# Kernel optimization log

Measured on AMD Instinct MI355X. Metric: run time of the kernel, lower is better.

Reference implementation:

```python
import jax, jax.numpy as jnp
import numpy as np

N_WAY, N_SHOT, C, H, W = 5, 5, 640, 32, 32
EPS = 1e-12


def conv1x1(x, w, b):
    # 1x1 conv == channel GEMM; w: (C_out, C_in), b: (C_out,)
    return jnp.einsum('bchw,oc->bohw', x, w) + b[None, :, None, None]


def setup_inputs() -> dict:
    key = jax.random.key(0)
    ks = jax.random.split(key, 7)
    B = N_WAY * N_SHOT
    x5 = jax.random.normal(ks[0], (B, C, H, W), jnp.float32)
    Wc = jax.random.normal(ks[1], (C, C), jnp.float32) * 0.02
    bc = jax.random.normal(ks[2], (C,), jnp.float32) * 0.02
    Wq = jax.random.normal(ks[3], (C, C), jnp.float32) * 0.02
    bq = jax.random.normal(ks[4], (C,), jnp.float32) * 0.02
    Wk = jax.random.normal(ks[5], (C, C), jnp.float32) * 0.02
    bk = jax.random.normal(ks[6], (C,), jnp.float32) * 0.02
    return {"x5": x5, "Wc": Wc, "bc": bc, "Wq": Wq, "bq": bq, "Wk": Wk, "bk": bk}


def reference(x5, Wc, bc, Wq, bq, Wk, bk):
    B, Cc, Hh, Ww = x5.shape
    HW = Hh * Ww
    scale = 1.0 / (Cc ** 0.5)

    # residual 1x1 conv, then query_transform applied once (x5 is reassigned)
    x5 = conv1x1(x5, Wc, bc) + x5
    x5 = conv1x1(x5, Wq, bq)

    # query: query_transform applied AGAIN on the already-transformed x5
    xq = conv1x1(x5, Wq, bq).reshape(N_WAY, N_SHOT, Cc, HW)
    xq = xq.transpose(0, 1, 3, 2).reshape(N_WAY, N_SHOT * HW, Cc)
    xk = conv1x1(x5, Wk, bk).reshape(N_WAY, N_SHOT, Cc, HW)
    xk = xk.transpose(0, 2, 1, 3).reshape(N_WAY, Cc, N_SHOT * HW)

    # QK scores per way: (n_way, S*HW, S*HW)
    xw = jnp.matmul(xq, xk) * scale
    # max over key spatial, mean over key shot
    xw = xw.reshape(N_WAY, N_SHOT * HW, N_SHOT, HW).max(-1).mean(-1)
    xw = jax.nn.softmax(xw.reshape(N_WAY, N_SHOT, HW), axis=-1)

    # channel-wise L2 normalize (F.normalize semantics)
    nrm = jnp.maximum(jnp.sqrt((x5 * x5).sum(1, keepdims=True)), EPS)
    norm0 = (x5 / nrm).reshape(N_WAY, N_SHOT, Cc, Hh, Ww)

    # argmax-equality mask over spatial positions
    xw_max = xw.max(-1, keepdims=True)
    mask = (xw == xw_max).astype(x5.dtype).reshape(N_WAY, N_SHOT, 1, Hh, Ww)

    # seeds: masked spatial sum of normalized features -> (n_way, n_shot, C)
    seeds = (norm0 * mask).sum((3, 4))

    # conv3d correlation: out[b,o,h,w] = sum_{k,c} norm0[b,k,c,h,w] * seeds[o,k,c]
    cm = jnp.einsum('bkchw,okc->bohw', norm0, seeds).reshape(N_WAY, N_WAY, HW)
    cmin = cm.min(-1, keepdims=True)
    cmax = cm.max(-1, keepdims=True)
    cm = (cm - cmin) / (cmax - cmin + EPS)
    cormap = cm.reshape(B, 1, Hh, Ww)

    x51 = (x5 * cormap).reshape(N_WAY, N_SHOT, Cc, Hh, Ww)
    proto1 = x51.mean((1, 3, 4))  # (n_way, C)
    return proto1
```

## Files before the change

### kernel.cpp

```cpp
#include <hip/hip_runtime.h>
#include <math.h>

#define NW 5
#define NS 5
#define CDIM 640
#define HWDIM 1024
#define BDIM 25
constexpr int CHW = CDIM * HWDIM;
constexpr int NBIG = BDIM * CHW;
constexpr int WSZ = CDIM * CDIM;
constexpr float QK_SCALE = 0.03952847075210474f;

typedef __attribute__((ext_vector_type(4))) float f32x4;
typedef __attribute__((ext_vector_type(8))) __bf16 bf16x8;
typedef __attribute__((ext_vector_type(4))) __bf16 bf16x4;
typedef __attribute__((ext_vector_type(2))) __bf16 bf16x2;

__device__ __forceinline__ void load_lds16(const __bf16* g, __bf16* l) {
    __builtin_amdgcn_global_load_lds(
        (const __attribute__((address_space(1))) void*)g,
        (__attribute__((address_space(3))) void*)l, 16, 0, 0);
}

__global__ __launch_bounds__(256) void split_f32(const float* __restrict__ s,
                                                 __bf16* __restrict__ dH,
                                                 __bf16* __restrict__ dL, int n4) {
    int i = blockIdx.x * 256 + threadIdx.x;
    if (i >= n4) return;
    f32x4 v = reinterpret_cast<const f32x4*>(s)[i];
    bf16x4 h, lo;
    #pragma unroll
    for (int q = 0; q < 4; ++q) {
        __bf16 hh = (__bf16)v[q];
        h[q] = hh;
        lo[q] = (__bf16)(v[q] - (float)hh);
    }
    reinterpret_cast<bf16x4*>(dH)[i] = h;
    reinterpret_cast<bf16x4*>(dL)[i] = lo;
}

__global__ __launch_bounds__(256) void tsplit(const float* __restrict__ x,
                                              __bf16* __restrict__ dH,
                                              __bf16* __restrict__ dL) {
    __shared__ float sT[32][33];
    const int hw0 = blockIdx.x * 32, c0 = blockIdx.y * 32, b = blockIdx.z;
    const int t = threadIdx.x;
    const int r = t >> 3, q4 = (t & 7) * 4;
    f32x4 v = *reinterpret_cast<const f32x4*>(
        &x[(size_t)b * CHW + (size_t)(c0 + r) * HWDIM + hw0 + q4]);
    #pragma unroll
    for (int i = 0; i < 4; ++i) sT[r][q4 + i] = v[i];
    __syncthreads();
    bf16x4 h, lo;
    #pragma unroll
    for (int i = 0; i < 4; ++i) {
        float xv = sT[q4 + i][r];
        __bf16 hh = (__bf16)xv;
        h[i] = hh;
        lo[i] = (__bf16)(xv - (float)hh);
    }
    size_t off = (size_t)b * CHW + (size_t)(hw0 + r) * CDIM + c0 + q4;
    *reinterpret_cast<bf16x4*>(&dH[off]) = h;
    *reinterpret_cast<bf16x4*>(&dL[off]) = lo;
}

__global__ __launch_bounds__(256) void wtsplit(const float* __restrict__ W,
                                               __bf16* __restrict__ dH,
                                               __bf16* __restrict__ dL) {
    __shared__ float sT[32][33];
    const int ci0 = blockIdx.x * 32, t0 = blockIdx.y * 32;
    const int t = threadIdx.x;
    const int r = t >> 3, q4 = (t & 7) * 4;
    f32x4 v = *reinterpret_cast<const f32x4*>(&W[(size_t)(t0 + r) * CDIM + ci0 + q4]);
    #pragma unroll
    for (int i = 0; i < 4; ++i) sT[r][q4 + i] = v[i];
    __syncthreads();
    bf16x4 h, lo;
    #pragma unroll
    for (int i = 0; i < 4; ++i) {
        float xv = sT[q4 + i][r];
        if (t0 + q4 + i == ci0 + r) xv += 1.0f;
        __bf16 hh = (__bf16)xv;
        h[i] = hh;
        lo[i] = (__bf16)(xv - (float)hh);
    }
    size_t off = (size_t)(ci0 + r) * CDIM + t0 + q4;
    *reinterpret_cast<bf16x4*>(&dH[off]) = h;
    *reinterpret_cast<bf16x4*>(&dL[off]) = lo;
}

__global__ void zero_k(float* __restrict__ p) { p[threadIdx.x] = 0.0f; }

__global__ void bias1_k(const float* __restrict__ Wq, const float* __restrict__ bc,
                        const float* __restrict__ bq, float* __restrict__ B2) {
    const int o = threadIdx.x;
    float s = bq[o];
    for (int t = 0; t < CDIM; ++t) s = fmaf(Wq[(size_t)o * CDIM + t], bc[t], s);
    B2[o] = s;
}

template <int NL>
__device__ __forceinline__ void stage_rows(const __bf16* __restrict__ srcH,
                                           const __bf16* __restrict__ srcL,
                                           __bf16* lds, int wv, int l, int c0) {
    const int lch = (l & 7) ^ (l >> 3);
    const int scol = (lch & 3) * 8;
    const int srw = l >> 3;
    const __bf16* src = (lch & 4) ? srcL : srcH;
    #pragma unroll
    for (int i = 0; i < NL; ++i) {
        const int r0 = wv * (8 * NL) + i * 8;
        load_lds16(&src[(size_t)(r0 + srw) * CDIM + c0 + scol], &lds[r0 * 64]);
    }
}

__global__ __launch_bounds__(256) void gemm_sm(
    const __bf16* __restrict__ inH, const __bf16* __restrict__ inL,
    const __bf16* __restrict__ wH, const __bf16* __restrict__ wL,
    const float* __restrict__ bias,
    __bf16* __restrict__ outH, __bf16* __restrict__ outL) {
    __shared__ __bf16 sA[128 * 64];
    __shared__ __bf16 sB[128 * 64];
    const int hw0 = blockIdx.x * 128;
    const int o0 = blockIdx.y * 128;
    const int tid = threadIdx.x;
    const int wv = tid >> 6, l = tid & 63;
    const int wo = (wv >> 1) * 64, wh = (wv & 1) * 64;

    const __bf16* wSrcH = wH + (size_t)o0 * CDIM;
    const __bf16* wSrcL = wL + (size_t)o0 * CDIM;
    const __bf16* iSrcH = inH + (size_t)hw0 * CDIM;
    const __bf16* iSrcL = inL + (size_t)hw0 * CDIM;

    f32x4 acc[4][4];
    #pragma unroll
    for (int i = 0; i < 4; ++i)
        #pragma unroll
        for (int j = 0; j < 4; ++j) acc[i][j] = (f32x4){0.f, 0.f, 0.f, 0.f};

    const int fr = l & 15, cf = l >> 4;
    const int ehi = (cf ^ (fr & 7)) * 8;

    for (int c0 = 0; c0 < CDIM; c0 += 32) {
        stage_rows<4>(wSrcH, wSrcL, sA, wv, l, c0);
        stage_rows<4>(iSrcH, iSrcL, sB, wv, l, c0);
        __syncthreads();
        bf16x8 aH[4], aL[4], bH[4], bL[4];
        #pragma unroll
        for (int i = 0; i < 4; ++i) {
            const int ra = (wo + i * 16 + fr) * 64;
            const int rb = (wh + i * 16 + fr) * 64;
            aH[i] = *reinterpret_cast<const bf16x8*>(&sA[ra + ehi]);
            aL[i] = *reinterpret_cast<const bf16x8*>(&sA[ra + (ehi ^ 32)]);
            bH[i] = *reinterpret_cast<const bf16x8*>(&sB[rb + ehi]);
            bL[i] = *reinterpret_cast<const bf16x8*>(&sB[rb + (ehi ^ 32)]);
        }
        #pragma unroll
        for (int i = 0; i < 4; ++i)
            #pragma unroll
            for (int j = 0; j < 4; ++j) {
                acc[i][j] = __builtin_amdgcn_mfma_f32_16x16x32_bf16(
                    aH[i], bH[j], acc[i][j], 0, 0, 0);
                acc[i][j] = __builtin_amdgcn_mfma_f32_16x16x32_bf16(
                    aH[i], bL[j], acc[i][j], 0, 0, 0);
                acc[i][j] = __builtin_amdgcn_mfma_f32_16x16x32_bf16(
                    aL[i], bH[j], acc[i][j], 0, 0, 0);
            }
        __syncthreads();
    }

    const int og = (l >> 4) * 4;
    const int cl = l & 15;
    #pragma unroll
    for (int i = 0; i < 4; ++i) {
        const int o = o0 + wo + i * 16 + og;
        const f32x4 bs = *reinterpret_cast<const f32x4*>(&bias[o]);
        #pragma unroll
        for (int j = 0; j < 4; ++j) {
            const int hw = hw0 + wh + j * 16 + cl;
            const size_t off = (size_t)hw * CDIM + o;
            bf16x4 oh, ol;
            #pragma unroll
            for (int q = 0; q < 4; ++q) {
                float r = acc[i][j][q] + bs[q];
                __bf16 hh = (__bf16)r;
                oh[q] = hh;
                ol[q] = (__bf16)(r - (float)hh);
            }
            *reinterpret_cast<bf16x4*>(&outH[off]) = oh;
            *reinterpret_cast<bf16x4*>(&outL[off]) = ol;
        }
    }
}

__global__ __launch_bounds__(256, 2) void conv_big(
    const __bf16* __restrict__ inH, const __bf16* __restrict__ inL,
    const __bf16* __restrict__ A0h, const __bf16* __restrict__ A0l,
    const __bf16* __restrict__ A1h, const __bf16* __restrict__ A1l,
    const float* __restrict__ bias,
    __bf16* __restrict__ O0h, __bf16* __restrict__ O0l,
    __bf16* __restrict__ O1h, __bf16* __restrict__ O1l) {
    __shared__ __bf16 sA[128 * 64];
    __shared__ __bf16 sB[256 * 64];
    const int hw0 = blockIdx.x * 256;
    const int oy = blockIdx.y;
    const int seg = oy / 5;
    const int o0 = (oy % 5) * 128;
    const int b = blockIdx.z;
    const int tid = threadIdx.x;
    const int wv = tid >> 6, l = tid & 63;
    const int wo = (wv >> 1) * 64;
    const int wh = (wv & 1) * 128;
    const size_t inBase = (size_t)b * CHW;

    const __bf16* Ah = seg ? A1h : A0h;
    const __bf16* Al = seg ? A1l : A0l;
    __bf16* OhP = seg ? O1h : O0h;
    __bf16* OlP = seg ? O1l : O0l;
    const __bf16* aSrcH = Ah + (size_t)o0 * CDIM;
    const __bf16* aSrcL = Al + (size_t)o0 * CDIM;
    const __bf16* bSrcH = inH + inBase + (size_t)hw0 * CDIM;
    const __bf16* bSrcL = inL + inBase + (size_t)hw0 * CDIM;

    f32x4 acc[4][8];
    #pragma unroll
    for (int i = 0; i < 4; ++i)
        #pragma unroll
        for (int j = 0; j < 8; ++j) acc[i][j] = (f32x4){0.f, 0.f, 0.f, 0.f};

    const int fr = l & 15, cf = l >> 4;
    const int ehi = (cf ^ (fr & 7)) * 8;

    for (int c0 = 0; c0 < CDIM; c0 += 32) {
        stage_rows<4>(aSrcH, aSrcL, sA, wv, l, c0);
        stage_rows<8>(bSrcH, bSrcL, sB, wv, l, c0);
        __syncthreads();
        bf16x8 aH[4], aL[4];
        #pragma unroll
        for (int i = 0; i < 4; ++i) {
            const int ra = (wo + i * 16 + fr) * 64;
            aH[i] = *reinterpret_cast<const bf16x8*>(&sA[ra + ehi]);
            aL[i] = *reinterpret_cast<const bf16x8*>(&sA[ra + (ehi ^ 32)]);
        }
        #pragma unroll
        for (int jh = 0; jh < 2; ++jh) {
            bf16x8 bH[4], bL[4];
            #pragma unroll
            for (int jj = 0; jj < 4; ++jj) {
                const int rb = (wh + (jh * 4 + jj) * 16 + fr) * 64;
                bH[jj] = *reinterpret_cast<const bf16x8*>(&sB[rb + ehi]);
                bL[jj] = *reinterpret_cast<const bf16x8*>(&sB[rb + (ehi ^ 32)]);
            }
            #pragma unroll
            for (int i = 0; i < 4; ++i)
                #pragma unroll
                for (int jj = 0; jj < 4; ++jj) {
                    const int j = jh * 4 + jj;
                    acc[i][j] = __builtin_amdgcn_mfma_f32_16x16x32_bf16(
                        aH[i], bH[jj], acc[i][j], 0, 0, 0);
                    acc[i][j] = __builtin_amdgcn_mfma_f32_16x16x32_bf16(
                        aH[i], bL[jj], acc[i][j], 0, 0, 0);
                    acc[i][j] = __builtin_amdgcn_mfma_f32_16x16x32_bf16(
                        aL[i], bH[jj], acc[i][j], 0, 0, 0);
                }
        }
        __syncthreads();
    }

    const int og = (l >> 4) * 4;
    const int cl = l & 15;
    #pragma unroll
    for (int i = 0; i < 4; ++i) {
        const int oLoc = o0 + wo + i * 16 + og;
        const f32x4 bs = *reinterpret_cast<const f32x4*>(&bias[oy * 128 + wo + i * 16 + og]);
        #pragma unroll
        for (int j = 0; j < 8; ++j) {
            const int hw = hw0 + wh + j * 16 + cl;
            const size_t off = inBase + (size_t)hw * CDIM + oLoc;
            bf16x4 oh, ol;
            #pragma unroll
            for (int q = 0; q < 4; ++q) {
                float r = acc[i][j][q] + bs[q];
                __bf16 hh = (__bf16)r;
                oh[q] = hh;
                ol[q] = (__bf16)(r - (float)hh);
            }
            *reinterpret_cast<bf16x4*>(&OhP[off]) = oh;
            *reinterpret_cast<bf16x4*>(&OlP[off]) = ol;
        }
    }
}

__global__ __launch_bounds__(256, 2) void attn_mfma2(
    const __bf16* __restrict__ qH, const __bf16* __restrict__ qL,
    const __bf16* __restrict__ kH, const __bf16* __restrict__ kL,
    float* __restrict__ gpart) {
    __shared__ __bf16 sQ[128 * 64];
    __shared__ __bf16 sK[256 * 64];
    __shared__ float sRed[2][128];
    const int qt = blockIdx.x;
    const int ks = blockIdx.y, wy = blockIdx.z;
    const int sq = qt >> 3, q0 = (qt & 7) * 128;
    const int tid = threadIdx.x;
    const int wv = tid >> 6, l = tid & 63;
    const int wq = (wv >> 1) * 64;
    const int kh = wv & 1;
    const int wk = kh * 128;
    const __bf16* qSrcH = qH + (size_t)(wy * NS + sq) * CHW + (size_t)q0 * CDIM;
    const __bf16* qSrcL = qL + (size_t)(wy * NS + sq) * CHW + (size_t)q0 * CDIM;
    const __bf16* kBaseH = kH + (size_t)(wy * NS + ks) * CHW;
    const __bf16* kBaseL = kL + (size_t)(wy * NS + ks) * CHW;

    float qmax[4][4];
    #pragma unroll
    for (int i = 0; i < 4; ++i)
        #pragma unroll
        for (int q = 0; q < 4; ++q) qmax[i][q] = -INFINITY;

    const int fr = l & 15, cf = l >> 4;
    const int ehi = (cf ^ (fr & 7)) * 8;

    for (int kc = 0; kc < 4; ++kc) {
        const __bf16* kSrcH = kBaseH + (size_t)(kc * 256) * CDIM;
        const __bf16* kSrcL = kBaseL + (size_t)(kc * 256) * CDIM;
        f32x4 acc[4][8];
        #pragma unroll
        for (int i = 0; i < 4; ++i)
            #pragma unroll
            for (int j = 0; j < 8; ++j) acc[i][j] = (f32x4){0.f, 0.f, 0.f, 0.f};

        for (int c0 = 0; c0 < CDIM; c0 += 32) {
            stage_rows<4>(qSrcH, qSrcL, sQ, wv, l, c0);
            stage_rows<8>(kSrcH, kSrcL, sK, wv, l, c0);
            __syncthreads();
            bf16x8 aH[4], aL[4];
            #pragma unroll
            for (int i = 0; i < 4; ++i) {
                const int ra = (wq + i * 16 + fr) * 64;
                aH[i] = *reinterpret_cast<const bf16x8*>(&sQ[ra + ehi]);
                aL[i] = *reinterpret_cast<const bf16x8*>(&sQ[ra + (ehi ^ 32)]);
            }
            __builtin_amdgcn_s_setprio(1);
            #pragma unroll
            for (int jh = 0; jh < 2; ++jh) {
                bf16x8 bH[4], bL[4];
                #pragma unroll
                for (int jj = 0; jj < 4; ++jj) {
                    const int rb = (wk + (jh * 4 + jj) * 16 + fr) * 64;
                    bH[jj] = *reinterpret_cast<const bf16x8*>(&sK[rb + ehi]);
                    bL[jj] = *reinterpret_cast<const bf16x8*>(&sK[rb + (ehi ^ 32)]);
                }
                #pragma unroll
                for (int i = 0; i < 4; ++i)
                    #pragma unroll
                    for (int jj = 0; jj < 4; ++jj) {
                        const int j = jh * 4 + jj;
                        acc[i][j] = __builtin_amdgcn_mfma_f32_16x16x32_bf16(
                            aH[i], bH[jj], acc[i][j], 0, 0, 0);
                        acc[i][j] = __builtin_amdgcn_mfma_f32_16x16x32_bf16(
                            aH[i], bL[jj], acc[i][j], 0, 0, 0);
                        acc[i][j] = __builtin_amdgcn_mfma_f32_16x16x32_bf16(
                            aL[i], bH[jj], acc[i][j], 0, 0, 0);
                    }
            }
            __builtin_amdgcn_s_setprio(0);
            __syncthreads();
        }
        #pragma unroll
        for (int i = 0; i < 4; ++i)
            #pragma unroll
            for (int q = 0; q < 4; ++q) {
                float m = acc[i][0][q];
                #pragma unroll
                for (int j = 1; j < 8; ++j) m = fmaxf(m, acc[i][j][q]);
                qmax[i][q] = fmaxf(qmax[i][q], m);
            }
    }
    #pragma unroll
    for (int i = 0; i < 4; ++i)
        #pragma unroll
        for (int q = 0; q < 4; ++q) {
            float v = qmax[i][q];
            v = fmaxf(v, __shfl_xor(v, 1));
            v = fmaxf(v, __shfl_xor(v, 2));
            v = fmaxf(v, __shfl_xor(v, 4));
            v = fmaxf(v, __shfl_xor(v, 8));
            qmax[i][q] = v;
        }
    if ((l & 15) == 0) {
        const int g = l >> 4;
        #pragma unroll
        for (int i = 0; i < 4; ++i)
            #pragma unroll
            for (int q = 0; q < 4; ++q)
                sRed[kh][wq + i * 16 + g * 4 + q] = qmax[i][q];
    }
    __syncthreads();
    if (tid < 128) {
        float m = fmaxf(sRed[0][tid], sRed[1][tid]);
        gpart[(size_t)(wy * NS + ks) * (NS * HWDIM) + sq * HWDIM + q0 + tid] =
            m * QK_SCALE;
    }
}

__global__ __launch_bounds__(256) void softmax_mask(const float* __restrict__ gpart,
                                                    int* __restrict__ gIdx,
                                                    int* __restrict__ gCnt) {
    const int bb = blockIdx.x;
    const int w = bb / NS, sq = bb % NS;
    const int tid = threadIdx.x;
    __shared__ float sred[256];
    __shared__ int sCnt;

    float v[4];
    #pragma unroll
    for (int i = 0; i < 4; ++i) {
        int hw = tid + 256 * i;
        float s = 0.f;
        #pragma unroll
        for (int ks = 0; ks < NS; ++ks)
            s += gpart[(size_t)(w * NS + ks) * (NS * HWDIM) + sq * HWDIM + hw];
        v[i] = s * 0.2f;
    }
    float m = fmaxf(fmaxf(v[0], v[1]), fmaxf(v[2], v[3]));
    sred[tid] = m;
    __syncthreads();
    for (int s = 128; s > 0; s >>= 1) {
        if (tid < s) sred[tid] = fmaxf(sred[tid], sred[tid + s]);
        __syncthreads();
    }
    float rowmax = sred[0];
    __syncthreads();
    float e[4], ls = 0.f;
    #pragma unroll
    for (int i = 0; i < 4; ++i) { e[i] = expf(v[i] - rowmax); ls += e[i]; }
    sred[tid] = ls;
    __syncthreads();
    for (int s = 128; s > 0; s >>= 1) {
        if (tid < s) sred[tid] += sred[tid + s];
        __syncthreads();
    }
    float ssum = sred[0];
    __syncthreads();
    float p[4], pm = 0.f;
    #pragma unroll
    for (int i = 0; i < 4; ++i) { p[i] = e[i] / ssum; pm = fmaxf(pm, p[i]); }
    sred[tid] = pm;
    __syncthreads();
    for (int s = 128; s > 0; s >>= 1) {
        if (tid < s) sred[tid] = fmaxf(sred[tid], sred[tid + s]);
        __syncthreads();
    }
    float pmax = sred[0];
    if (tid == 0) sCnt = 0;
    __syncthreads();
    #pragma unroll
    for (int i = 0; i < 4; ++i) {
        if (p[i] == pmax) {
            int slot = atomicAdd(&sCnt, 1);
            gIdx[bb * HWDIM + slot] = tid + 256 * i;
        }
    }
    __syncthreads();
    if (tid == 0) gCnt[bb] = sCnt;
}

__global__ __launch_bounds__(256) void nrm_k(const __bf16* __restrict__ yH,
                                             const __bf16* __restrict__ yL,
                                             float* __restrict__ inv) {
    const int row = blockIdx.x * 16 + (threadIdx.x >> 4);
    const int cq = threadIdx.x & 15;
    const size_t base = (size_t)row * CDIM;
    float s = 0.f;
    #pragma unroll
    for (int i = 0; i < 10; ++i) {
        int c = i * 64 + cq * 4;
        bf16x4 h = *reinterpret_cast<const bf16x4*>(&yH[base + c]);
        bf16x4 lo = *reinterpret_cast<const bf16x4*>(&yL[base + c]);
        #pragma unroll
        for (int q = 0; q < 4; ++q) {
            float x = (float)h[q] + (float)lo[q];
            s = fmaf(x, x, s);
        }
    }
    s += __shfl_xor(s, 1);
    s += __shfl_xor(s, 2);
    s += __shfl_xor(s, 4);
    s += __shfl_xor(s, 8);
    if (cq == 0) inv[row] = 1.0f / fmaxf(sqrtf(s), 1e-12f);
}

__global__ __launch_bounds__(640) void seeds_k(const __bf16* __restrict__ yH,
                                               const __bf16* __restrict__ yL,
                                               const float* __restrict__ inv,
                                               const int* __restrict__ gIdx,
                                               const int* __restrict__ gCnt,
                                               float* __restrict__ seeds) {
    const int bb = blockIdx.x, c = threadIdx.x;
    const int cnt = gCnt[bb];
    float s = 0.f;
    for (int e = 0; e < cnt; ++e) {
        int hw = gIdx[bb * HWDIM + e];
        size_t off = (size_t)bb * CHW + (size_t)hw * CDIM + c;
        s += ((float)yH[off] + (float)yL[off]) * inv[bb * HWDIM + hw];
    }
    seeds[bb * CDIM + c] = s;
}

__global__ __launch_bounds__(256) void cm_k(const __bf16* __restrict__ yH,
                                            const __bf16* __restrict__ yL,
                                            const float* __restrict__ inv,
                                            const float* __restrict__ seeds,
                                            float* __restrict__ cm) {
    __shared__ float sS[BDIM * CDIM];
    const int way = blockIdx.y;
    const int tid = threadIdx.x, wv = tid >> 6, l = tid & 63;
    const int hw = blockIdx.x * 4 + wv;
    for (int e = tid; e < BDIM * CDIM; e += 256) sS[e] = seeds[e];
    __syncthreads();
    float acc[NW] = {0.f, 0.f, 0.f, 0.f, 0.f};
    for (int k = 0; k < NS; ++k) {
        const size_t base = (size_t)(way * NS + k) * CHW + (size_t)hw * CDIM;
        float t[NW] = {0.f, 0.f, 0.f, 0.f, 0.f};
        #pragma unroll
        for (int i = 0; i < 5; ++i) {
            int c = (i * 64 + l) * 2;
            bf16x2 h = *reinterpret_cast<const bf16x2*>(&yH[base + c]);
            bf16x2 lo = *reinterpret_cast<const bf16x2*>(&yL[base + c]);
            float x0 = (float)h[0] + (float)lo[0];
            float x1 = (float)h[1] + (float)lo[1];
            #pragma unroll
            for (int o = 0; o < NW; ++o) {
                t[o] = fmaf(x0, sS[(o * NS + k) * CDIM + c], t[o]);
                t[o] = fmaf(x1, sS[(o * NS + k) * CDIM + c + 1], t[o]);
            }
        }
        float iv = inv[(way * NS + k) * HWDIM + hw];
        #pragma unroll
        for (int o = 0; o < NW; ++o) acc[o] = fmaf(t[o], iv, acc[o]);
    }
    #pragma unroll
    for (int o = 0; o < NW; ++o) {
        float v = acc[o];
        v += __shfl_xor(v, 1);
        v += __shfl_xor(v, 2);
        v += __shfl_xor(v, 4);
        v += __shfl_xor(v, 8);
        v += __shfl_xor(v, 16);
        v += __shfl_xor(v, 32);
        if (l == 0) cm[(size_t)(way * NW + o) * HWDIM + hw] = v;
    }
}

__global__ __launch_bounds__(256) void minmax_kernel(float* __restrict__ cm) {
    const int row = blockIdx.x;
    const int tid = threadIdx.x;
    __shared__ float smn[256], smx[256];
    float v[4];
    #pragma unroll
    for (int i = 0; i < 4; ++i) v[i] = cm[(size_t)row * HWDIM + tid + 256 * i];
    float mn = fminf(fminf(v[0], v[1]), fminf(v[2], v[3]));
    float mx = fmaxf(fmaxf(v[0], v[1]), fmaxf(v[2], v[3]));
    smn[tid] = mn;
    smx[tid] = mx;
    __syncthreads();
    for (int s = 128; s > 0; s >>= 1) {
        if (tid < s) {
            smn[tid] = fminf(smn[tid], smn[tid + s]);
            smx[tid] = fmaxf(smx[tid], smx[tid + s]);
        }
        __syncthreads();
    }
    float cmin = smn[0], cmax = smx[0];
    float den = cmax - cmin + 1e-12f;
    #pragma unroll
    for (int i = 0; i < 4; ++i)
        cm[(size_t)row * HWDIM + tid + 256 * i] = (v[i] - cmin) / den;
}

__global__ __launch_bounds__(128) void proto_part_k(const __bf16* __restrict__ yH,
                                                    const __bf16* __restrict__ yL,
                                                    const float* __restrict__ cmn,
                                                    float* __restrict__ part) {
    const int w = blockIdx.x, cc = blockIdx.y, hs = blockIdx.z;
    const int c = cc * 128 + threadIdx.x;
    float s = 0.f;
    for (int i = 0; i < 640; ++i) {
        int g = hs * 640 + i, sh = g >> 10, hw = g & 1023;
        size_t off = (size_t)(w * NS + sh) * CHW + (size_t)hw * CDIM + c;
        s = fmaf((float)yH[off] + (float)yL[off],
                 cmn[(w * NS + sh) * HWDIM + hw], s);
    }
    part[((w * 5 + cc) * 8 + hs) * 128 + threadIdx.x] = s;
}

__global__ __launch_bounds__(128) void proto_red_k(const float* __restrict__ part,
                                                   float* __restrict__ out) {
    const int bid = blockIdx.x;
    float s = 0.f;
    #pragma unroll
    for (int hs = 0; hs < 8; ++hs) s += part[(bid * 8 + hs) * 128 + threadIdx.x];
    const int w = bid / 5, cc = bid % 5;
    out[w * CDIM + cc * 128 + threadIdx.x] = s * (1.0f / 5120.0f);
}

extern "C" void kernel_launch(void* const* d_in, const int* in_sizes, int n_in,
                              void* d_out, int out_size, void* d_ws, size_t ws_size,
                              hipStream_t stream) {
    const float* x5 = (const float*)d_in[0];
    const float* Wc = (const float*)d_in[1];
    const float* bc = (const float*)d_in[2];
    const float* Wq = (const float*)d_in[3];
    const float* bq = (const float*)d_in[4];
    const float* Wk = (const float*)d_in[5];
    const float* bk = (const float*)d_in[6];
    float* out = (float*)d_out;

    __bf16* big = (__bf16*)d_ws;
    __bf16* Ah = big;
    __bf16* Al = big + (size_t)NBIG;
    __bf16* Bh = big + (size_t)2 * NBIG;
    __bf16* Bl = big + (size_t)3 * NBIG;
    __bf16* W2H = Bh;
    __bf16* W2L = Bh + WSZ;
    __bf16* Ch = big + (size_t)4 * NBIG;
    __bf16* Cl = big + (size_t)5 * NBIG;
    __bf16* WcTH = Ch;
    __bf16* WcTL = Ch + WSZ;
    __bf16* wp = big + (size_t)6 * NBIG;
    __bf16* WqH = wp;
    __bf16* WqL = wp + WSZ;
    __bf16* WkH = wp + 2 * WSZ;
    __bf16* WkL = wp + 3 * WSZ;
    float* fp = (float*)(wp + 4 * WSZ);
    float* zbias = fp;
    float* B2 = fp + 640;
    float* bb2 = fp + 1280;
    float* gpart = fp + 2560;
    float* invb = gpart + 128000;
    float* seedsb = invb + 25600;
    float* cmb = seedsb + 16000;
    float* partb = cmb + 25600;
    int* gIdx = (int*)(partb + 25600);
    int* gCnt = gIdx + BDIM * HWDIM;

    const int W4 = WSZ / 4;
    split_f32<<<dim3((W4 + 255) / 256), 256, 0, stream>>>(Wq, WqH, WqL, W4);
    split_f32<<<dim3((W4 + 255) / 256), 256, 0, stream>>>(Wk, WkH, WkL, W4);
    wtsplit<<<dim3(20, 20), 256, 0, stream>>>(Wc, WcTH, WcTL);
    tsplit<<<dim3(32, 20, 25), 256, 0, stream>>>(x5, Ah, Al);
    zero_k<<<1, 640, 0, stream>>>(zbias);
    bias1_k<<<1, 640, 0, stream>>>(Wq, bc, bq, B2);
    hipMemcpyAsync(bb2, bq, CDIM * sizeof(float), hipMemcpyDeviceToDevice, stream);
    hipMemcpyAsync(bb2 + CDIM, bk, CDIM * sizeof(float), hipMemcpyDeviceToDevice,
                   stream);

    gemm_sm<<<dim3(5, 5, 1), 256, 0, stream>>>(WqH, WqL, WcTH, WcTL, zbias,
                                               W2H, W2L);
    conv_big<<<dim3(4, 5, 25), 256, 0, stream>>>(Ah, Al, W2H, W2L, W2H, W2L,
                                                 B2, Ch, Cl, Ch, Cl);
    conv_big<<<dim3(4, 10, 25), 256, 0, stream>>>(Ch, Cl, WqH, WqL, WkH, WkL,
                                                  bb2, Ah, Al, Bh, Bl);

    attn_mfma2<<<dim3(40, 5, 5), 256, 0, stream>>>(Ah, Al, Bh, Bl, gpart);
    softmax_mask<<<25, 256, 0, stream>>>(gpart, gIdx, gCnt);
    nrm_k<<<1600, 256, 0, stream>>>(Ch, Cl, invb);
    seeds_k<<<25, 640, 0, stream>>>(Ch, Cl, invb, gIdx, gCnt, seedsb);
    cm_k<<<dim3(256, 5), 256, 0, stream>>>(Ch, Cl, invb, seedsb, cmb);
    minmax_kernel<<<25, 256, 0, stream>>>(cmb);
    proto_part_k<<<dim3(5, 5, 8), 128, 0, stream>>>(Ch, Cl, cmb, partb);
    proto_red_k<<<25, 128, 0, stream>>>(partb, out);
}
```

Before: 1.007 ms.

## Screen QK max with single bf16 MFMA pass, then refine candidates exactly

The QK score pass now uses only the high bf16 parts (1 MFMA per tile instead of 3). It records key candidates whose approximate score lies within an error bound of the running row max, where the bound comes from query and key norms. A refine kernel then recomputes exact dot products only for those candidates, falling back to a full scan when a row overflows. This cuts MFMA work in the dominant attention kernel, at the cost of extra norm kernels, atomics and a gather-style refine pass. Correctness depends on the heuristic error coefficient bounding the bf16 rounding error. Small bias and memcpy launches are also merged into one kernel.

```diff
diff --git a/kernel.cpp b/kernel.cpp
--- a/kernel.cpp
+++ b/kernel.cpp
@@ -6,10 +6,13 @@
 #define CDIM 640
 #define HWDIM 1024
 #define BDIM 25
+#define CAP 24
 constexpr int CHW = CDIM * HWDIM;
 constexpr int NBIG = BDIM * CHW;
 constexpr int WSZ = CDIM * CDIM;
+constexpr int NROWS = NW * NS * NS * HWDIM;
 constexpr float QK_SCALE = 0.03952847075210474f;
+constexpr float TWOE_COEF = 0.016f;
 
 typedef __attribute__((ext_vector_type(4))) float f32x4;
 typedef __attribute__((ext_vector_type(8))) __bf16 bf16x8;
@@ -89,14 +92,17 @@
     *reinterpret_cast<bf16x4*>(&dL[off]) = lo;
 }
 
-__global__ void zero_k(float* __restrict__ p) { p[threadIdx.x] = 0.0f; }
-
-__global__ void bias1_k(const float* __restrict__ Wq, const float* __restrict__ bc,
-                        const float* __restrict__ bq, float* __restrict__ B2) {
+__global__ void bias_prep(const float* __restrict__ Wq, const float* __restrict__ bc,
+                          const float* __restrict__ bq, const float* __restrict__ bk,
+                          float* __restrict__ zbias, float* __restrict__ B2,
+                          float* __restrict__ bb2) {
     const int o = threadIdx.x;
+    zbias[o] = 0.0f;
     float s = bq[o];
     for (int t = 0; t < CDIM; ++t) s = fmaf(Wq[(size_t)o * CDIM + t], bc[t], s);
     B2[o] = s;
+    bb2[o] = bq[o];
+    bb2[CDIM + o] = bk[o];
 }
 
 template <int NL>
@@ -112,6 +118,16 @@
         const int r0 = wv * (8 * NL) + i * 8;
         load_lds16(&src[(size_t)(r0 + srw) * CDIM + c0 + scol], &lds[r0 * 64]);
     }
+}
+
+__device__ __forceinline__ void stage_hi(const __bf16* __restrict__ src,
+                                         __bf16* lds, int li, int l) {
+    const int rp = li * 8 + (l >> 3);
+    const int pc = l & 7;
+    const int lc = pc ^ (rp & 7);
+    const int srow = 2 * rp + (lc >> 2);
+    const int schan = (lc & 3) * 8;
+    load_lds16(&src[(size_t)srow * CDIM + schan], &lds[li * 512]);
 }
 
 __global__ __launch_bounds__(256) void gemm_sm(
@@ -291,13 +307,66 @@
     }
 }
 
-__global__ __launch_bounds__(256, 2) void attn_mfma2(
-    const __bf16* __restrict__ qH, const __bf16* __restrict__ qL,
-    const __bf16* __restrict__ kH, const __bf16* __restrict__ kL,
-    float* __restrict__ gpart) {
-    __shared__ __bf16 sQ[128 * 64];
-    __shared__ __bf16 sK[256 * 64];
-    __shared__ float sRed[2][128];
+__global__ __launch_bounds__(256) void qknorm_k(const __bf16* __restrict__ xqH,
+                                                const __bf16* __restrict__ xqL,
+                                                const __bf16* __restrict__ xkH,
+                                                const __bf16* __restrict__ xkL,
+                                                float* __restrict__ qn,
+                                                float* __restrict__ knrow) {
+    const int gb = blockIdx.x;
+    const __bf16 *H, *L;
+    float* dst;
+    int row;
+    if (gb < 1600) {
+        H = xqH; L = xqL; dst = qn;
+        row = gb * 16 + (threadIdx.x >> 4);
+    } else {
+        H = xkH; L = xkL; dst = knrow;
+        row = (gb - 1600) * 16 + (threadIdx.x >> 4);
+    }
+    const int cq = threadIdx.x & 15;
+    const size_t base = (size_t)row * CDIM;
+    float s = 0.f;
+    #pragma unroll
+    for (int i = 0; i < 10; ++i) {
+        int c = i * 64 + cq * 4;
+        bf16x4 h = *reinterpret_cast<const bf16x4*>(&H[base + c]);
+        bf16x4 lo = *reinterpret_cast<const bf16x4*>(&L[base + c]);
+        #pragma unroll
+        for (int q = 0; q < 4; ++q) {
+            float x = (float)h[q] + (float)lo[q];
+            s = fmaf(x, x, s);
+        }
+    }
+    s += __shfl_xor(s, 1);
+    s += __shfl_xor(s, 2);
+    s += __shfl_xor(s, 4);
+    s += __shfl_xor(s, 8);
+    if (cq == 0) dst[row] = sqrtf(s);
+}
+
+__global__ __launch_bounds__(256) void kmax_k(const float* __restrict__ knrow,
+                                              float* __restrict__ kmax) {
+    const int b = blockIdx.x, tid = threadIdx.x;
+    __shared__ float sm[256];
+    const float* p = knrow + b * 1024;
+    float v = fmaxf(fmaxf(p[tid], p[tid + 256]), fmaxf(p[tid + 512], p[tid + 768]));
+    sm[tid] = v;
+    __syncthreads();
+    for (int s = 128; s > 0; s >>= 1) {
+        if (tid < s) sm[tid] = fmaxf(sm[tid], sm[tid + s]);
+        __syncthreads();
+    }
+    if (tid == 0) kmax[b] = sm[0];
+}
+
+__global__ __launch_bounds__(256, 2) void attn_bf16(
+    const __bf16* __restrict__ qH, const __bf16* __restrict__ kH,
+    const float* __restrict__ qn, const float* __restrict__ kmax,
+    int* __restrict__ candCnt, unsigned short* __restrict__ candIdx) {
+    __shared__ __bf16 sQ[64 * 64];
+    __shared__ __bf16 sK[128 * 64];
+    __shared__ float sM[2][128];
     const int qt = blockIdx.x;
     const int ks = blockIdx.y, wy = blockIdx.z;
     const int sq = qt >> 3, q0 = (qt & 7) * 128;
@@ -306,23 +375,31 @@
     const int wq = (wv >> 1) * 64;
     const int kh = wv & 1;
     const int wk = kh * 128;
-    const __bf16* qSrcH = qH + (size_t)(wy * NS + sq) * CHW + (size_t)q0 * CDIM;
-    const __bf16* qSrcL = qL + (size_t)(wy * NS + sq) * CHW + (size_t)q0 * CDIM;
-    const __bf16* kBaseH = kH + (size_t)(wy * NS + ks) * CHW;
-    const __bf16* kBaseL = kL + (size_t)(wy * NS + ks) * CHW;
-
-    float qmax[4][4];
+    const __bf16* qSrc = qH + (size_t)(wy * NS + sq) * CHW + (size_t)q0 * CDIM;
+    const __bf16* kBase = kH + (size_t)(wy * NS + ks) * CHW;
+
+    const int fr = l & 15, cg = l >> 4;
+    const int rowBase = ((wy * NS + ks) * NS + sq) * HWDIM + q0;
+
+    const float kmv = kmax[wy * NS + ks];
+    float twoE[4][4];
+    float run[4][4];
     #pragma unroll
     for (int i = 0; i < 4; ++i)
         #pragma unroll
-        for (int q = 0; q < 4; ++q) qmax[i][q] = -INFINITY;
-
-    const int fr = l & 15, cf = l >> 4;
-    const int ehi = (cf ^ (fr & 7)) * 8;
+        for (int qq = 0; qq < 4; ++qq) {
+            int qloc = wq + i * 16 + (cg << 2) + qq;
+            twoE[i][qq] = TWOE_COEF * qn[(wy * NS + sq) * HWDIM + q0 + qloc] * kmv + 1e-6f;
+            run[i][qq] = -INFINITY;
+        }
+
+    const int rq2 = fr >> 1, par = fr & 1;
+    const int xorm = rq2 & 7;
+    const int cA = (wq / 2 + rq2) * 64 + (((par << 2) | cg) ^ xorm) * 8;
+    const int cB = (wk / 2 + rq2) * 64 + (((par << 2) | cg) ^ xorm) * 8;
 
     for (int kc = 0; kc < 4; ++kc) {
-        const __bf16* kSrcH = kBaseH + (size_t)(kc * 256) * CDIM;
-        const __bf16* kSrcL = kBaseL + (size_t)(kc * 256) * CDIM;
+        const __bf16* kSrc = kBase + (size_t)(kc * 256) * CDIM;
         f32x4 acc[4][8];
         #pragma unroll
         for (int i = 0; i < 4; ++i)
@@ -330,77 +407,128 @@
             for (int j = 0; j < 8; ++j) acc[i][j] = (f32x4){0.f, 0.f, 0.f, 0.f};
 
         for (int c0 = 0; c0 < CDIM; c0 += 32) {
-            stage_rows<4>(qSrcH, qSrcL, sQ, wv, l, c0);
-            stage_rows<8>(kSrcH, kSrcL, sK, wv, l, c0);
+            stage_hi(qSrc + c0, sQ, wv * 2 + 0, l);
+            stage_hi(qSrc + c0, sQ, wv * 2 + 1, l);
+            #pragma unroll
+            for (int li = 0; li < 4; ++li) stage_hi(kSrc + c0, sK, wv * 4 + li, l);
             __syncthreads();
-            bf16x8 aH[4], aL[4];
-            #pragma unroll
-            for (int i = 0; i < 4; ++i) {
-                const int ra = (wq + i * 16 + fr) * 64;
-                aH[i] = *reinterpret_cast<const bf16x8*>(&sQ[ra + ehi]);
-                aL[i] = *reinterpret_cast<const bf16x8*>(&sQ[ra + (ehi ^ 32)]);
-            }
+            bf16x8 aH[4], bH[8];
+            #pragma unroll
+            for (int i = 0; i < 4; ++i)
+                aH[i] = *reinterpret_cast<const bf16x8*>(&sQ[cA + i * 512]);
+            #pragma unroll
+            for (int j = 0; j < 8; ++j)
+                bH[j] = *reinterpret_cast<const bf16x8*>(&sK[cB + j * 512]);
             __builtin_amdgcn_s_setprio(1);
             #pragma unroll
-            for (int jh = 0; jh < 2; ++jh) {
-                bf16x8 bH[4], bL[4];
+            for (int i = 0; i < 4; ++i)
                 #pragma unroll
-                for (int jj = 0; jj < 4; ++jj) {
-                    const int rb = (wk + (jh * 4 + jj) * 16 + fr) * 64;
-                    bH[jj] = *reinterpret_cast<const bf16x8*>(&sK[rb + ehi]);
-                    bL[jj] = *reinterpret_cast<const bf16x8*>(&sK[rb + (ehi ^ 32)]);
-                }
-                #pragma unroll
-                for (int i = 0; i < 4; ++i)
-                    #pragma unroll
-                    for (int jj = 0; jj < 4; ++jj) {
-                        const int j = jh * 4 + jj;
-                        acc[i][j] = __builtin_amdgcn_mfma_f32_16x16x32_bf16(
-                            aH[i], bH[jj], acc[i][j], 0, 0, 0);
-                        acc[i][j] = __builtin_amdgcn_mfma_f32_16x16x32_bf16(
-                            aH[i], bL[jj], acc[i][j], 0, 0, 0);
-                        acc[i][j] = __builtin_amdgcn_mfma_f32_16x16x32_bf16(
-                            aL[i], bH[jj], acc[i][j], 0, 0, 0);
-                    }
-            }
+                for (int j = 0; j < 8; ++j)
+                    acc[i][j] = __builtin_amdgcn_mfma_f32_16x16x32_bf16(
+                        aH[i], bH[j], acc[i][j], 0, 0, 0);
             __builtin_amdgcn_s_setprio(0);
             __syncthreads();
         }
         #pragma unroll
         for (int i = 0; i < 4; ++i)
             #pragma unroll
-            for (int q = 0; q < 4; ++q) {
-                float m = acc[i][0][q];
+            for (int qq = 0; qq < 4; ++qq) {
+                float m = acc[i][0][qq];
                 #pragma unroll
-                for (int j = 1; j < 8; ++j) m = fmaxf(m, acc[i][j][q]);
-                qmax[i][q] = fmaxf(qmax[i][q], m);
+                for (int j = 1; j < 8; ++j) m = fmaxf(m, acc[i][j][qq]);
+                m = fmaxf(m, __shfl_xor(m, 1));
+                m = fmaxf(m, __shfl_xor(m, 2));
+                m = fmaxf(m, __shfl_xor(m, 4));
+                m = fmaxf(m, __shfl_xor(m, 8));
+                if (fr == 0)
+                    sM[kh][wq + i * 16 + (cg << 2) + qq] = m;
             }
-    }
-    #pragma unroll
-    for (int i = 0; i < 4; ++i)
-        #pragma unroll
-        for (int q = 0; q < 4; ++q) {
-            float v = qmax[i][q];
-            v = fmaxf(v, __shfl_xor(v, 1));
-            v = fmaxf(v, __shfl_xor(v, 2));
-            v = fmaxf(v, __shfl_xor(v, 4));
-            v = fmaxf(v, __shfl_xor(v, 8));
-            qmax[i][q] = v;
-        }
-    if ((l & 15) == 0) {
-        const int g = l >> 4;
+        __syncthreads();
         #pragma unroll
         for (int i = 0; i < 4; ++i)
             #pragma unroll
-            for (int q = 0; q < 4; ++q)
-                sRed[kh][wq + i * 16 + g * 4 + q] = qmax[i][q];
-    }
-    __syncthreads();
-    if (tid < 128) {
-        float m = fmaxf(sRed[0][tid], sRed[1][tid]);
-        gpart[(size_t)(wy * NS + ks) * (NS * HWDIM) + sq * HWDIM + q0 + tid] =
-            m * QK_SCALE;
-    }
+            for (int qq = 0; qq < 4; ++qq) {
+                const int rloc = wq + i * 16 + (cg << 2) + qq;
+                run[i][qq] = fmaxf(run[i][qq],
+                                   fmaxf(sM[0][rloc], sM[1][rloc]));
+                const float th = run[i][qq] - twoE[i][qq];
+                const int rowid = rowBase + rloc;
+                #pragma unroll
+                for (int j = 0; j < 8; ++j) {
+                    if (acc[i][j][qq] >= th) {
+                        int key = kc * 256 + wk + j * 16 + fr;
+                        int slot = atomicAdd(&candCnt[rowid], 1);
+                        if (slot < CAP)
+                            candIdx[rowid * CAP + slot] = (unsigned short)key;
+                    }
+                }
+            }
+    }
+}
+
+__global__ __launch_bounds__(256) void refine_k(
+    const __bf16* __restrict__ qH, const __bf16* __restrict__ qL,
+    const __bf16* __restrict__ kH, const __bf16* __restrict__ kL,
+    const int* __restrict__ candCnt, const unsigned short* __restrict__ candIdx,
+    float* __restrict__ gpart) {
+    const int tid = threadIdx.x, wv = tid >> 6, l = tid & 63;
+    const int rowid = blockIdx.x * 4 + wv;
+    const int wks = rowid / (NS * HWDIM);
+    const int rem = rowid - wks * (NS * HWDIM);
+    const int sq = rem >> 10, qp = rem & 1023;
+    const int w = wks / NS;
+    const __bf16* qh = qH + (size_t)(w * NS + sq) * CHW + (size_t)qp * CDIM;
+    const __bf16* ql = qL + (size_t)(w * NS + sq) * CHW + (size_t)qp * CDIM;
+    const __bf16* kb = kH + (size_t)wks * CHW;
+    const __bf16* kbl = kL + (size_t)wks * CHW;
+
+    float qv[10];
+    #pragma unroll
+    for (int e = 0; e < 10; ++e) {
+        int c = l * 10 + e;
+        qv[e] = (float)qh[c] + (float)ql[c];
+    }
+    const int cnt = candCnt[rowid];
+    float smax = -INFINITY;
+    if (cnt <= CAP) {
+        for (int e = 0; e < cnt; ++e) {
+            const int key = candIdx[rowid * CAP + e];
+            const __bf16* kr = kb + (size_t)key * CDIM;
+            const __bf16* krl = kbl + (size_t)key * CDIM;
+            float s = 0.f;
+            #pragma unroll
+            for (int u = 0; u < 10; ++u) {
+                int c = l * 10 + u;
+                s = fmaf(qv[u], (float)kr[c] + (float)krl[c], s);
+            }
+            s += __shfl_xor(s, 1);
+            s += __shfl_xor(s, 2);
+            s += __shfl_xor(s, 4);
+            s += __shfl_xor(s, 8);
+            s += __shfl_xor(s, 16);
+            s += __shfl_xor(s, 32);
+            smax = fmaxf(smax, s);
+        }
+    } else {
+        for (int key = 0; key < 1024; ++key) {
+            const __bf16* kr = kb + (size_t)key * CDIM;
+            const __bf16* krl = kbl + (size_t)key * CDIM;
+            float s = 0.f;
+            #pragma unroll
+            for (int u = 0; u < 10; ++u) {
+                int c = l * 10 + u;
+                s = fmaf(qv[u], (float)kr[c] + (float)krl[c], s);
+            }
+            s += __shfl_xor(s, 1);
+            s += __shfl_xor(s, 2);
+            s += __shfl_xor(s, 4);
+            s += __shfl_xor(s, 8);
+            s += __shfl_xor(s, 16);
+            s += __shfl_xor(s, 32);
+            smax = fmaxf(smax, s);
+        }
+    }
+    if (l == 0) gpart[rowid] = smax * QK_SCALE;
 }
 
 __global__ __launch_bounds__(256) void softmax_mask(const float* __restrict__ gpart,
@@ -641,19 +769,21 @@
     float* seedsb = invb + 25600;
     float* cmb = seedsb + 16000;
     float* partb = cmb + 25600;
-    int* gIdx = (int*)(partb + 25600);
+    float* qn = partb + 25600;
+    float* knrow = qn + 25600;
+    float* kmaxb = knrow + 25600;
+    int* gIdx = (int*)(kmaxb + 32);
     int* gCnt = gIdx + BDIM * HWDIM;
+    int* candCnt = gCnt + 32;
+    unsigned short* candIdx = (unsigned short*)(candCnt + NROWS);
 
     const int W4 = WSZ / 4;
     split_f32<<<dim3((W4 + 255) / 256), 256, 0, stream>>>(Wq, WqH, WqL, W4);
     split_f32<<<dim3((W4 + 255) / 256), 256, 0, stream>>>(Wk, WkH, WkL, W4);
     wtsplit<<<dim3(20, 20), 256, 0, stream>>>(Wc, WcTH, WcTL);
     tsplit<<<dim3(32, 20, 25), 256, 0, stream>>>(x5, Ah, Al);
-    zero_k<<<1, 640, 0, stream>>>(zbias);
-    bias1_k<<<1, 640, 0, stream>>>(Wq, bc, bq, B2);
-    hipMemcpyAsync(bb2, bq, CDIM * sizeof(float), hipMemcpyDeviceToDevice, stream);
-    hipMemcpyAsync(bb2 + CDIM, bk, CDIM * sizeof(float), hipMemcpyDeviceToDevice,
-                   stream);
+    bias_prep<<<1, 640, 0, stream>>>(Wq, bc, bq, bk, zbias, B2, bb2);
+    hipMemsetAsync(candCnt, 0, NROWS * sizeof(int), stream);
 
     gemm_sm<<<dim3(5, 5, 1), 256, 0, stream>>>(WqH, WqL, WcTH, WcTL, zbias,
                                                W2H, W2L);
@@ -662,7 +792,12 @@
     conv_big<<<dim3(4, 10, 25), 256, 0, stream>>>(Ch, Cl, WqH, WqL, WkH, WkL,
                                                   bb2, Ah, Al, Bh, Bl);
 
-    attn_mfma2<<<dim3(40, 5, 5), 256, 0, stream>>>(Ah, Al, Bh, Bl, gpart);
+    qknorm_k<<<3200, 256, 0, stream>>>(Ah, Al, Bh, Bl, qn, knrow);
+    kmax_k<<<25, 256, 0, stream>>>(knrow, kmaxb);
+    attn_bf16<<<dim3(40, 5, 5), 256, 0, stream>>>(Ah, Bh, qn, kmaxb,
+                                                  candCnt, candIdx);
+    refine_k<<<NROWS / 4, 256, 0, stream>>>(Ah, Al, Bh, Bl, candCnt, candIdx,
+                                            gpart);
     softmax_mask<<<25, 256, 0, stream>>>(gpart, gIdx, gCnt);
     nrm_k<<<1600, 256, 0, stream>>>(Ch, Cl, invb);
     seeds_k<<<25, 640, 0, stream>>>(Ch, Cl, invb, gIdx, gCnt, seedsb);
```

After: 1.774 ms. 76.1% more time.
